# Optimization experiments

Hardware: AMD Instinct MI355X
Metric: run time of the kernel (lower is better)

## Reference

```python
import jax, jax.numpy as jnp
import numpy as np

B, T, C = 2, 2048, 1024
H = 16
D = C // H
SCALE = 0.1 / (D ** 0.5)  # nonstandard 0.1/sqrt(head_dim) scale from source


def setup_inputs() -> dict:
    key = jax.random.key(0)
    ks = jax.random.split(key, 5)
    s = 0.02
    return {
        "x": jax.random.normal(ks[0], (B, T, C), jnp.float32),
        "w_attn": jax.random.normal(ks[1], (C, 3 * C), jnp.float32) * s,
        "b_attn": jax.random.normal(ks[2], (3 * C,), jnp.float32) * s,
        "w_proj": jax.random.normal(ks[3], (C, C), jnp.float32) * s,
        "b_proj": jax.random.normal(ks[4], (C,), jnp.float32) * s,
    }


def reference(x, w_attn, b_attn, w_proj, b_proj):
    Bs, Ts, Cs = x.shape
    qkv = x @ w_attn + b_attn                      # [B,T,3C]
    q, k, v = jnp.split(qkv, 3, axis=-1)
    q = q.reshape(Bs, Ts, H, D)                    # [B,T,H,D]
    k = k.reshape(Bs, Ts, H, D)
    v = v.reshape(Bs, Ts, H, D)
    attn = jnp.einsum("bthd,bshd->bhts", q, k) * SCALE  # [B,H,T,T]
    causal = jnp.tril(jnp.ones((Ts, Ts), dtype=bool))
    attn = jnp.where(causal, attn, -jnp.inf)
    attn = jax.nn.softmax(attn, axis=-1)
    y = jnp.einsum("bhts,bshd->bthd", attn, v).reshape(Bs, Ts, Cs)
    return y @ w_proj + b_proj
```

## Files before the change

kernel.cpp:

```cpp
#include <hip/hip_runtime.h>


#define Bz 2
#define Tz 2048
#define Cz 1024
#define Hz 16
#define Dz 64
#define QSCALE 0.01803368801111437f

typedef unsigned short u16;
typedef short bf16x4 __attribute__((ext_vector_type(4)));
typedef short bf16x8 __attribute__((ext_vector_type(8)));
typedef float f32x4 __attribute__((ext_vector_type(4)));

#define MFMA32(A, B, C) __builtin_amdgcn_mfma_f32_16x16x32_bf16(A, B, C, 0, 0, 0)

__device__ inline f32x4 mfma16(bf16x4 a, bf16x4 b, f32x4 c) {
#if defined(__HIP_DEVICE_COMPILE__)
  return __builtin_amdgcn_mfma_f32_16x16x16bf16_1k(a, b, c, 0, 0, 0);
#else
  return c;
#endif
}

__device__ inline u16 f2bf(float f) {
  return (u16)((__float_as_uint(f) + 0x8000u) >> 16);
}

__device__ inline float fexp2(float x) {
#if __has_builtin(__builtin_amdgcn_exp2f)
  return __builtin_amdgcn_exp2f(x);
#else
  return exp2f(x);
#endif
}

__device__ inline void gl_lds16(const u16* g, u16* l) {
  __builtin_amdgcn_global_load_lds(
      (const __attribute__((address_space(1))) void*)g,
      (__attribute__((address_space(3))) void*)l, 16, 0, 0);
}

#define NCAST 4096
#define NTA   3072
__global__ __launch_bounds__(256) void prep_kernel(const float* __restrict__ x,
                                                   const float* __restrict__ wa,
                                                   const float* __restrict__ wp,
                                                   u16* __restrict__ xb,
                                                   u16* __restrict__ waT,
                                                   u16* __restrict__ wpT) {
  const int bx = blockIdx.x, t = threadIdx.x;
  if (bx < NCAST) {
    int i = bx * 256 + t;
    float4 v = ((const float4*)x)[i];
    ushort4 o = {f2bf(v.x), f2bf(v.y), f2bf(v.z), f2bf(v.w)};
    ((ushort4*)xb)[i] = o;
    return;
  }
  __shared__ float tile[32][33];
  const float* W;
  u16* WT;
  int N, idx;
  if (bx < NCAST + NTA) {
    W = wa; WT = waT; N = 3 * Cz; idx = bx - NCAST;
  } else {
    W = wp; WT = wpT; N = Cz; idx = bx - NCAST - NTA;
  }
  const int n0 = (idx % (N / 32)) * 32, k0 = (idx / (N / 32)) * 32;
  const int tx = t & 31, ty = t >> 5;
#pragma unroll
  for (int i = 0; i < 4; ++i)
    tile[ty + 8 * i][tx] = W[(size_t)(k0 + ty + 8 * i) * N + n0 + tx];
  __syncthreads();
#pragma unroll
  for (int i = 0; i < 4; ++i)
    WT[(size_t)(n0 + ty + 8 * i) * Cz + k0 + tx] = f2bf(tile[tx][ty + 8 * i]);
}

template <bool OUT_BF16, int TN, bool VSPLIT>
__global__ __launch_bounds__(256) void gemm_bt(const u16* __restrict__ A,
                                               const u16* __restrict__ BT,
                                               const float* __restrict__ bias,
                                               void* __restrict__ Cout,
                                               u16* __restrict__ vTout,
                                               int M, int N, int K,
                                               int qcols, float qscale) {
  __shared__ __align__(16) u16 As[128 * 64];
  __shared__ __align__(16) u16 Bs[TN * 64];
  constexpr int NT = TN / 32;
  const int t = threadIdx.x;
  const int wave = t >> 6, lane = t & 63;
  const int lm = lane & 15, lg = lane >> 4;
  const int wm = wave >> 1, wn = wave & 1;
  const int m0 = blockIdx.y * 128, n0 = blockIdx.x * TN;

  const int lrow = lane >> 3;
  const int gseg = (lane & 7) ^ lrow;
  const size_t a_base = (size_t)(m0 + 32 * wave + lrow) * K + gseg * 8;
  u16* const a_lds = &As[(32 * wave) * 64];
  const size_t b_base = (size_t)(n0 + (TN / 4) * wave + lrow) * K + gseg * 8;
  u16* const b_lds = &Bs[((TN / 4) * wave) * 64];

  f32x4 acc[4][NT];
#pragma unroll
  for (int mt = 0; mt < 4; ++mt)
#pragma unroll
    for (int nt = 0; nt < NT; ++nt)
#pragma unroll
      for (int i = 0; i < 4; ++i) acc[mt][nt][i] = 0.f;

  for (int k0 = 0; k0 < K; k0 += 64) {
    __syncthreads();
#pragma unroll
    for (int i = 0; i < 4; ++i)
      gl_lds16(A + a_base + (size_t)(8 * i) * K + k0, a_lds + i * 8 * 64);
#pragma unroll
    for (int i = 0; i < NT; ++i)
      gl_lds16(BT + b_base + (size_t)(8 * i) * K + k0, b_lds + i * 8 * 64);
    __syncthreads();

#pragma unroll
    for (int h = 0; h < 2; ++h) {
      const int rs = ((lg + 4 * h) ^ (lm & 7)) * 8;
      bf16x8 af[4], bfr[NT];
#pragma unroll
      for (int mt = 0; mt < 4; ++mt)
        af[mt] = *(const bf16x8*)&As[(64 * wm + 16 * mt + lm) * 64 + rs];
#pragma unroll
      for (int nt = 0; nt < NT; ++nt)
        bfr[nt] = *(const bf16x8*)&Bs[((TN / 2) * wn + 16 * nt + lm) * 64 + rs];
#pragma unroll
      for (int mt = 0; mt < 4; ++mt)
#pragma unroll
        for (int nt = 0; nt < NT; ++nt)
          acc[mt][nt] = MFMA32(af[mt], bfr[nt], acc[mt][nt]);
    }
  }

#pragma unroll
  for (int nt = 0; nt < NT; ++nt) {
    int gc = n0 + (TN / 2) * wn + 16 * nt + lm;
    float bv = bias[gc];
    if (VSPLIT && gc >= 2 * Cz) {
      const int dg = gc - 2 * Cz;
#pragma unroll
      for (int mt = 0; mt < 4; ++mt) {
        const int gr0 = m0 + 64 * wm + 16 * mt + 4 * lg;
        const int bb = gr0 >> 11, s0 = gr0 & 2047;
        ushort4 o = {f2bf(acc[mt][nt][0] + bv), f2bf(acc[mt][nt][1] + bv),
                     f2bf(acc[mt][nt][2] + bv), f2bf(acc[mt][nt][3] + bv)};
        *(ushort4*)(vTout + (((size_t)(bb * 1024 + dg)) << 11) + s0) = o;
      }
      continue;
    }
    float sc = (gc < qcols) ? qscale : 1.f;
#pragma unroll
    for (int mt = 0; mt < 4; ++mt) {
#pragma unroll
      for (int i = 0; i < 4; ++i) {
        int gr = m0 + 64 * wm + 16 * mt + 4 * lg + i;
        float v = (acc[mt][nt][i] + bv) * sc;
        if (OUT_BF16)
          ((u16*)Cout)[(size_t)gr * N + gc] = f2bf(v);
        else
          ((float*)Cout)[(size_t)gr * N + gc] = v;
      }
    }
  }
}

__global__ __launch_bounds__(256) void attn_kernel(const u16* __restrict__ qkv,
                                                   const u16* __restrict__ vT,
                                                   u16* __restrict__ yb) {
  __shared__ __align__(16) u16 KsL[2][64 * 64];
  __shared__ __align__(16) u16 VtL[2][64 * 64];

  const int t = threadIdx.x;
  const int wave = t >> 6, lane = t & 63;
  const int lm = lane & 15, lg = lane >> 4;
  const int x = blockIdx.x;
  const int bh = x & 31, qtp = x >> 5;
  const int qt = (qtp < 16) ? qtp : 47 - qtp;
  const int b = bh >> 4, h = bh & 15;
  const int q0 = qt * 64;
  const size_t rowstride = 3 * Cz;
  const u16* qbase = qkv + (size_t)b * Tz * rowstride + h * Dz;
  const u16* vTbh = vT + ((size_t)(b * Hz + h) * Dz) * Tz;

  bf16x8 qf[2];
  {
    const u16* qrow = qbase + (size_t)(q0 + wave * 16 + lm) * rowstride + (lg << 3);
    qf[0] = *(const bf16x8*)qrow;
    qf[1] = *(const bf16x8*)(qrow + 32);
  }

  float psum = 0.f;
  f32x4 Oa[4];
#pragma unroll
  for (int i = 0; i < 4; ++i)
#pragma unroll
    for (int j = 0; j < 4; ++j) Oa[i][j] = 0.f;

  const int srow = lane >> 3;
  const int sgl = ((lane & 7) ^ srow) * 8;
  const u16* kstg = qbase + Cz + (size_t)(16 * wave + srow) * rowstride + sgl;
  const u16* vstg = vTbh + (size_t)(16 * wave + srow) * Tz + sgl;

  auto stage_issue = [&](int kt, int buf) {
#pragma unroll
    for (int c2 = 0; c2 < 2; ++c2) {
      gl_lds16(kstg + (size_t)(8 * c2) * rowstride + (size_t)(64 * kt) * rowstride,
               &KsL[buf][(16 * wave + 8 * c2) * 64]);
      gl_lds16(vstg + (size_t)(8 * c2) * Tz + 64 * kt,
               &VtL[buf][(16 * wave + 8 * c2) * 64]);
    }
  };

  stage_issue(0, 0);

  for (int kt = 0; kt <= qt; ++kt) {
    __syncthreads();
    const int cb = kt & 1;
    if (kt + 1 <= qt) stage_issue(kt + 1, 1 - cb);

    f32x4 S[4];
#pragma unroll
    for (int c = 0; c < 4; ++c) {
      const int rb = (16 * c + lm) * 64;
      bf16x8 k0 = *(const bf16x8*)&KsL[cb][rb + ((lg ^ (lm & 7)) << 3)];
      bf16x8 k1 = *(const bf16x8*)&KsL[cb][rb + (((lg + 4) ^ (lm & 7)) << 3)];
      f32x4 s;
#pragma unroll
      for (int i = 0; i < 4; ++i) s[i] = 0.f;
      s = MFMA32(k0, qf[0], s);
      s = MFMA32(k1, qf[1], s);
      S[c] = s;
    }

    const bool diag = (kt == qt);
    const int qloc = 16 * wave + lm;
    bf16x4 pf[4];
#pragma unroll
    for (int c = 0; c < 4; ++c) {
#pragma unroll
      for (int r = 0; r < 4; ++r) {
        float p = fexp2(S[c][r]);
        if (diag && (c * 16 + 4 * lg + r) > qloc) p = 0.f;
        psum += p;
        pf[c][r] = (short)f2bf(p);
      }
    }

#pragma unroll
    for (int dt = 0; dt < 4; ++dt) {
      const int rb = (16 * dt + lm) * 64;
#pragma unroll
      for (int c = 0; c < 4; ++c) {
        const int off = (((2 * c + (lg >> 1)) ^ (lm & 7)) << 3) + 4 * (lg & 1);
        bf16x4 vfr = *(const bf16x4*)&VtL[cb][rb + off];
        Oa[dt] = mfma16(pf[c], vfr, Oa[dt]);
      }
    }
  }

  float s = psum;
  s += __shfl_xor(s, 16);
  s += __shfl_xor(s, 32);
  const float linv = 1.f / s;
  float invq[4];
#pragma unroll
  for (int r = 0; r < 4; ++r)
    invq[r] = __shfl(linv, 20 * lg + r);
  __syncthreads();
#pragma unroll
  for (int dt = 0; dt < 4; ++dt)
#pragma unroll
    for (int r = 0; r < 4; ++r)
      KsL[0][(16 * wave + 4 * lg + r) * 64 + 16 * dt + lm] =
          f2bf(Oa[dt][r] * invq[r]);
  __syncthreads();
  {
    const int row = lane >> 2, seg = lane & 3;
    const uint4* src = (const uint4*)&KsL[0][(16 * wave + row) * 64 + seg * 16];
    uint4 v0 = src[0];
    uint4 v1 = src[1];
    u16* dst = yb + (size_t)(b * Tz + q0 + 16 * wave + row) * Cz + h * Dz + seg * 16;
    *(uint4*)dst = v0;
    *(uint4*)(dst + 8) = v1;
  }
}

extern "C" void kernel_launch(void* const* d_in, const int* in_sizes, int n_in,
                              void* d_out, int out_size, void* d_ws, size_t ws_size,
                              hipStream_t stream) {
  const float* x      = (const float*)d_in[0];
  const float* w_attn = (const float*)d_in[1];
  const float* b_attn = (const float*)d_in[2];
  const float* w_proj = (const float*)d_in[3];
  const float* b_proj = (const float*)d_in[4];

  char* ws = (char*)d_ws;
  u16* xb   = (u16*)(ws);
  u16* waT  = (u16*)(ws + (8ull << 20));
  u16* wpT  = (u16*)(ws + (14ull << 20));
  u16* qkvb = (u16*)(ws + (16ull << 20));
  u16* yb   = (u16*)(ws + (40ull << 20));
  u16* vTt  = (u16*)(ws + (48ull << 20));

  const int M = Bz * Tz;

  prep_kernel<<<NCAST + NTA + 1024, 256, 0, stream>>>(x, w_attn, w_proj, xb, waT, wpT);
  gemm_bt<true, 128, true><<<dim3(3 * Cz / 128, M / 128), 256, 0, stream>>>(
      xb, waT, b_attn, qkvb, vTt, M, 3 * Cz, Cz, Cz, QSCALE);
  attn_kernel<<<1024, 256, 0, stream>>>(qkvb, vTt, yb);
  gemm_bt<false, 64, false><<<dim3(Cz / 64, M / 128), 256, 0, stream>>>(
      yb, wpT, b_proj, d_out, nullptr, M, Cz, Cz, 0, 1.f);
}
```

Before: 169.8 us.

## Add 256x256-tile pipelined QKV GEMM with swizzled LDS and phase-staged loads

Replaces the generic 128x128 QKV projection GEMM with a dedicated 512-thread kernel that computes a 256x256 output tile per block. It uses an XOR-swizzled, double-buffered LDS layout filled by direct global-to-LDS loads, issued in four quarter-tile phases that overlap with MFMA work, and raises wave priority around the MFMA bursts. The aim is more reuse per loaded byte and better hiding of load latency, at the cost of 128 KB of LDS and heavy register use, which limit occupancy. The grid shrinks to 192 blocks, which may underfill the GPU's compute units.

Result: slower. 177.6 us (+4.6%).

```diff
diff --git a/kernel.cpp b/kernel.cpp
--- a/kernel.cpp
+++ b/kernel.cpp
@@ -75,6 +75,126 @@
 #pragma unroll
   for (int i = 0; i < 4; ++i)
     WT[(size_t)(n0 + ty + 8 * i) * Cz + k0 + tx] = f2bf(tile[tx][ty + 8 * i]);
+}
+
+__global__ __launch_bounds__(512, 2) void gemm_qkv(const u16* __restrict__ A,
+                                                   const u16* __restrict__ BT,
+                                                   const float* __restrict__ bias,
+                                                   u16* __restrict__ Cout,
+                                                   u16* __restrict__ vTout) {
+  constexpr int K = Cz;
+  constexpr int N = 3 * Cz;
+  constexpr int KT = K / 64;
+  __shared__ __align__(16) u16 L[2][4][128 * 64];
+
+  const int t = threadIdx.x;
+  const int wave = t >> 6, lane = t & 63;
+  const int lm = lane & 15, lg = lane >> 4;
+  const int wm = wave >> 2, wn = wave & 3;
+  const int m0 = blockIdx.y * 256, n0 = blockIdx.x * 256;
+
+  const int srow = 8 * wave + (lane >> 3);
+  const int sgl = ((lane & 7) ^ (lane >> 3)) * 8;
+
+  auto stage_ht = [&](int kt, int ht) {
+    const bool isA = (ht == 0) || (ht == 3);
+    const int half = (ht >= 2) ? 1 : 0;
+    const u16* src =
+        (isA ? A + (size_t)(m0 + half * 128 + srow) * K
+             : BT + (size_t)(n0 + half * 128 + srow) * K) +
+        (size_t)kt * 64 + sgl;
+    u16* dst = &L[kt & 1][ht][(8 * wave) * 64];
+    gl_lds16(src, dst);
+    gl_lds16(src + (size_t)64 * K, dst + 64 * 64);
+  };
+
+  f32x4 acc[2][2][4][2];
+#pragma unroll
+  for (int qa = 0; qa < 2; ++qa)
+#pragma unroll
+    for (int qb = 0; qb < 2; ++qb)
+#pragma unroll
+      for (int mt = 0; mt < 4; ++mt)
+#pragma unroll
+        for (int nt = 0; nt < 2; ++nt)
+#pragma unroll
+          for (int i = 0; i < 4; ++i) acc[qa][qb][mt][nt][i] = 0.f;
+
+#pragma unroll
+  for (int i = 0; i < 4; ++i) stage_ht(0, i);
+  asm volatile("s_waitcnt vmcnt(4)" ::: "memory");
+  __builtin_amdgcn_s_barrier();
+
+  for (int kt = 0; kt < KT; ++kt) {
+    const int cb = kt & 1;
+#pragma unroll
+    for (int ph = 0; ph < 4; ++ph) {
+      const int qa = ph >> 1, qb = ph & 1;
+      bf16x8 af[4][2], bfr[2][2];
+#pragma unroll
+      for (int mt = 0; mt < 4; ++mt)
+#pragma unroll
+        for (int h = 0; h < 2; ++h)
+          af[mt][h] = *(const bf16x8*)&L[cb][qa ? 3 : 0]
+              [(64 * wm + 16 * mt + lm) * 64 + (((lg + 4 * h) ^ (lm & 7)) << 3)];
+#pragma unroll
+      for (int nt = 0; nt < 2; ++nt)
+#pragma unroll
+        for (int h = 0; h < 2; ++h)
+          bfr[nt][h] = *(const bf16x8*)&L[cb][qb ? 2 : 1]
+              [(32 * wn + 16 * nt + lm) * 64 + (((lg + 4 * h) ^ (lm & 7)) << 3)];
+      if (kt + 1 < KT) stage_ht(kt + 1, ph);
+      __builtin_amdgcn_s_barrier();
+      asm volatile("s_waitcnt lgkmcnt(0)" ::: "memory");
+      __builtin_amdgcn_s_setprio(1);
+#pragma unroll
+      for (int mt = 0; mt < 4; ++mt)
+#pragma unroll
+        for (int nt = 0; nt < 2; ++nt) {
+          acc[qa][qb][mt][nt] = MFMA32(af[mt][0], bfr[nt][0], acc[qa][qb][mt][nt]);
+          acc[qa][qb][mt][nt] = MFMA32(af[mt][1], bfr[nt][1], acc[qa][qb][mt][nt]);
+        }
+      __builtin_amdgcn_s_setprio(0);
+      if (kt < KT - 1)
+        asm volatile("s_waitcnt vmcnt(4)" ::: "memory");
+      else if (ph == 0)
+        asm volatile("s_waitcnt vmcnt(2)" ::: "memory");
+      else
+        asm volatile("s_waitcnt vmcnt(0)" ::: "memory");
+      __builtin_amdgcn_s_barrier();
+    }
+  }
+
+#pragma unroll
+  for (int qa = 0; qa < 2; ++qa)
+#pragma unroll
+    for (int qb = 0; qb < 2; ++qb)
+#pragma unroll
+      for (int nt = 0; nt < 2; ++nt) {
+        const int gc = n0 + 128 * qb + 32 * wn + 16 * nt + lm;
+        const float bv = bias[gc];
+        if (gc >= 2 * Cz) {
+          const int dg = gc - 2 * Cz;
+#pragma unroll
+          for (int mt = 0; mt < 4; ++mt) {
+            const int gr0 = m0 + 128 * qa + 64 * wm + 16 * mt + 4 * lg;
+            const int bb = gr0 >> 11, s0 = gr0 & 2047;
+            const f32x4 av = acc[qa][qb][mt][nt];
+            ushort4 o = {f2bf(av[0] + bv), f2bf(av[1] + bv),
+                         f2bf(av[2] + bv), f2bf(av[3] + bv)};
+            *(ushort4*)(vTout + (((size_t)(bb * 1024 + dg)) << 11) + s0) = o;
+          }
+        } else {
+          const float sc = (gc < Cz) ? QSCALE : 1.f;
+#pragma unroll
+          for (int mt = 0; mt < 4; ++mt)
+#pragma unroll
+            for (int i = 0; i < 4; ++i) {
+              const int gr = m0 + 128 * qa + 64 * wm + 16 * mt + 4 * lg + i;
+              Cout[(size_t)gr * N + gc] = f2bf((acc[qa][qb][mt][nt][i] + bv) * sc);
+            }
+        }
+      }
 }
 
 template <bool OUT_BF16, int TN, bool VSPLIT>
@@ -310,8 +430,7 @@
   const int M = Bz * Tz;
 
   prep_kernel<<<NCAST + NTA + 1024, 256, 0, stream>>>(x, w_attn, w_proj, xb, waT, wpT);
-  gemm_bt<true, 128, true><<<dim3(3 * Cz / 128, M / 128), 256, 0, stream>>>(
-      xb, waT, b_attn, qkvb, vTt, M, 3 * Cz, Cz, Cz, QSCALE);
+  gemm_qkv<<<dim3(3 * Cz / 256, M / 256), 512, 0, stream>>>(xb, waT, b_attn, qkvb, vTt);
   attn_kernel<<<1024, 256, 0, stream>>>(qkvb, vTt, yb);
   gemm_bt<false, 64, false><<<dim3(Cz / 64, M / 128), 256, 0, stream>>>(
       yb, wpT, b_proj, d_out, nullptr, M, Cz, Cz, 0, 1.f);
```
